# Kernel optimization log

Measured on AMD Instinct MI355X. Metric: run time of the kernel, lower is better.

Reference implementation:

```python
import jax, jax.numpy as jnp
import numpy as np

N, F_IN, HID, HEADS, NCLS, E = 50000, 512, 64, 4, 64, 800000
NEG_SLOPE = 0.2
EPS = 1e-16


def setup_inputs() -> dict:
    key = jax.random.key(0)
    ks = jax.random.split(key, 10)
    s = 0.1
    return {
        "x": jax.random.normal(ks[0], (N, F_IN), jnp.float32),
        "edge_index": jax.random.randint(ks[1], (2, E), 0, N, jnp.int64),
        "W1": jax.random.normal(ks[2], (F_IN, HEADS * HID), jnp.float32) * s,
        "a_src1": jax.random.normal(ks[3], (HEADS, HID), jnp.float32) * s,
        "a_dst1": jax.random.normal(ks[4], (HEADS, HID), jnp.float32) * s,
        "b1": jax.random.normal(ks[5], (HEADS * HID,), jnp.float32) * s,
        "W2": jax.random.normal(ks[6], (HEADS * HID, NCLS), jnp.float32) * s,
        "a_src2": jax.random.normal(ks[7], (1, NCLS), jnp.float32) * s,
        "a_dst2": jax.random.normal(ks[8], (1, NCLS), jnp.float32) * s,
        "b2": jax.random.normal(ks[9], (NCLS,), jnp.float32) * s,
    }


def gat_conv(x, W, a_src, a_dst, b, src, dst):
    H, C = a_src.shape
    h = (x @ W).reshape(-1, H, C)                     # [N, H, C]
    # per-node attention halves, gathered per edge -> [E', H]
    al_src = jnp.einsum("nhc,hc->nh", h, a_src)
    al_dst = jnp.einsum("nhc,hc->nh", h, a_dst)
    e = jax.nn.leaky_relu(al_src[src] + al_dst[dst], NEG_SLOPE)
    # segment softmax over destination neighborhoods
    m = jax.ops.segment_max(e, dst, num_segments=x.shape[0])
    ex = jnp.exp(e - m[dst])
    denom = jax.ops.segment_sum(ex, dst, num_segments=x.shape[0])
    alpha = ex / (denom[dst] + EPS)                   # [E', H]
    out = jax.ops.segment_sum(alpha[:, :, None] * h[src], dst,
                              num_segments=x.shape[0])  # [N, H, C]
    return out.reshape(-1, H * C) + b


def reference(x, edge_index, W1, a_src1, a_dst1, b1, W2, a_src2, a_dst2, b2):
    n = x.shape[0]
    loop = jnp.arange(n, dtype=edge_index.dtype)
    src = jnp.concatenate([edge_index[0], loop])       # add self loops (PyG default)
    dst = jnp.concatenate([edge_index[1], loop])
    h = gat_conv(x, W1, a_src1, a_dst1, b1, src, dst)
    h = jax.nn.elu(h)                                  # dropout is identity in eval
    out = gat_conv(h, W2, a_src2, a_dst2, b2, src, dst)
    return jax.nn.log_softmax(out, axis=1)
```

## Files before the change

### kernel.cpp

```cpp
#include <hip/hip_runtime.h>
#include <math.h>

#define F_IN 512
#define HC1 256
#define HEADS 4
#define HID 64
#define NCLS 64
#define NEG_SLOPE 0.2f
#define EPS_DENOM 1e-16f

using short8 = __attribute__((ext_vector_type(8))) short;
using f32x4  = __attribute__((ext_vector_type(4))) float;

__device__ inline float wave_sum(float v) {
#pragma unroll
  for (int s = 32; s > 0; s >>= 1) v += __shfl_xor(v, s);
  return v;
}

__device__ inline unsigned short f2bf(float f) {
  unsigned int u = __float_as_uint(f);
  u = (u + 0x7FFF + ((u >> 16) & 1)) >> 16;
  return (unsigned short)u;
}
__device__ inline float bflo(unsigned int u) { return __uint_as_float(u << 16); }
__device__ inline float bfhi(unsigned int u) { return __uint_as_float(u & 0xFFFF0000u); }

__device__ inline unsigned int cvtpk_bf16(float lo, float hi) {
  unsigned int r;
  asm("v_cvt_pk_bf16_f32 %0, %1, %2" : "=v"(r) : "v"(lo), "v"(hi));
  return r;
}

__device__ inline void async_copy16(const void* g, void* l) {
  __builtin_amdgcn_global_load_lds((const __attribute__((address_space(1))) void*)g,
                                   (__attribute__((address_space(3))) void*)l, 16, 0, 0);
}

__global__ void castT_kernel(const float* __restrict__ W, unsigned short* __restrict__ WT,
                             int K, int Nn) {
  int id = blockIdx.x * blockDim.x + threadIdx.x;
  if (id >= K * Nn) return;
  int n = id / K, k = id % K;
  WT[id] = f2bf(W[(size_t)k * Nn + n]);
}


__global__ void hist_kernel(const int* __restrict__ dst, int E, int* __restrict__ cnt) {
  int i = blockIdx.x * blockDim.x + threadIdx.x;
  int stride = gridDim.x * blockDim.x;
  for (int e = i; e < E; e += stride) atomicAdd(&cnt[dst[e]], 1);
}

__global__ void scan_blocks_kernel(const int* __restrict__ cnt, int n,
                                   int* __restrict__ rowoff, int* __restrict__ cursor,
                                   int* __restrict__ bsum) {
  __shared__ int wpart[16];
  int b = blockIdx.x, tid = threadIdx.x;
  int i = b * 1024 + tid;
  int lane = tid & 63, wid = tid >> 6;
  int v = (i < n) ? (cnt[i] + 1) : 0;
  int x = v;
#pragma unroll
  for (int s = 1; s < 64; s <<= 1) {
    int t = __shfl_up(x, s);
    if (lane >= s) x += t;
  }
  if (lane == 63) wpart[wid] = x;
  __syncthreads();
  if (wid == 0) {
    int p = (lane < 16) ? wpart[lane] : 0;
#pragma unroll
    for (int s = 1; s < 16; s <<= 1) {
      int t = __shfl_up(p, s);
      if (lane >= s) p += t;
    }
    if (lane < 16) wpart[lane] = p;
  }
  __syncthreads();
  int incl = x + (wid ? wpart[wid - 1] : 0);
  if (i < n) { rowoff[i + 1] = incl; cursor[i] = incl - v; }
  if (tid == 1023) bsum[b] = incl;
  if (b == 0 && tid == 0) rowoff[0] = 0;
}

__global__ void scan_partials_kernel(int* __restrict__ bsum, int nb) {
  int lane = threadIdx.x;
  int v = (lane < nb) ? bsum[lane] : 0;
  int x = v;
#pragma unroll
  for (int s = 1; s < 64; s <<= 1) {
    int t = __shfl_up(x, s);
    if (lane >= s) x += t;
  }
  if (lane < nb) bsum[lane] = x - v;
}

__global__ void scan_add_kernel(int n, int* __restrict__ rowoff, int* __restrict__ cursor,
                                const int* __restrict__ bsum) {
  int i = blockIdx.x * 1024 + threadIdx.x;
  int off = bsum[blockIdx.x];
  if (i < n) { rowoff[i + 1] += off; cursor[i] += off; }
}

__global__ void scatter_kernel(const int* __restrict__ src, const int* __restrict__ dst,
                               int E, int n, int* __restrict__ cursor, int* __restrict__ esrc) {
  int i = blockIdx.x * blockDim.x + threadIdx.x;
  int stride = gridDim.x * blockDim.x;
  for (int e = i; e < E + n; e += stride) {
    int s, d;
    if (e < E) { s = src[e]; d = dst[e]; } else { s = e - E; d = s; }
    int pos = atomicAdd(&cursor[d], 1);
    esrc[pos] = s;
  }
}


__global__ __launch_bounds__(256)
void gemm1_fused_kernel(const float* __restrict__ A, const unsigned short* __restrict__ BT,
                        unsigned short* __restrict__ Cb, int M) {
  constexpr int BM = 128, BN = 128, BK = 32, K = F_IN, Nn = HC1;
  __shared__ unsigned short Alds[BM * BK];
  __shared__ unsigned short Blds[BN * BK];
  const int t = threadIdx.x;
  const int lane = t & 63;
  const int w = t >> 6;
  const int wr = (w >> 1) * 64;
  const int wc = (w & 1) * 64;
  const int row0 = blockIdx.y * BM;
  const int col0 = blockIdx.x * BN;
  const int lrow = lane & 15;
  const int lk = (lane >> 4) * 8;

  f32x4 acc[4][4] = {};
  const int ar = t >> 1;
  const int kh = (t & 1) * 16;
  int grow = row0 + ar; if (grow > M - 1) grow = M - 1;
  const float* arow = A + (size_t)grow * K + kh;

  for (int k0 = 0; k0 < K; k0 += BK) {
#pragma unroll
    for (int i = 0; i < 2; ++i) {
      int c = i * 256 + t;
      int br = c >> 2;
      int bk = (c & 3) * 8;
      const unsigned short* g = BT + (size_t)(col0 + br) * K + k0 + bk;
      unsigned short* l = Blds + (size_t)(i * 256 + w * 64) * 8;
      async_copy16(g, l);
    }
    const float4* gp = (const float4*)(arow + k0);
    float4 f0 = gp[0], f1 = gp[1], f2 = gp[2], f3 = gp[3];
    uint4 u0, u1;
    u0.x = cvtpk_bf16(f0.x, f0.y); u0.y = cvtpk_bf16(f0.z, f0.w);
    u0.z = cvtpk_bf16(f1.x, f1.y); u0.w = cvtpk_bf16(f1.z, f1.w);
    u1.x = cvtpk_bf16(f2.x, f2.y); u1.y = cvtpk_bf16(f2.z, f2.w);
    u1.z = cvtpk_bf16(f3.x, f3.y); u1.w = cvtpk_bf16(f3.z, f3.w);
    uint4* dstp = (uint4*)&Alds[ar * BK + kh];
    dstp[0] = u0; dstp[1] = u1;
    __syncthreads();
    short8 a[4], b[4];
#pragma unroll
    for (int m = 0; m < 4; ++m)
      a[m] = *(const short8*)&Alds[(wr + m * 16 + lrow) * BK + lk];
#pragma unroll
    for (int n = 0; n < 4; ++n)
      b[n] = *(const short8*)&Blds[(wc + n * 16 + lrow) * BK + lk];
#pragma unroll
    for (int m = 0; m < 4; ++m)
#pragma unroll
      for (int n = 0; n < 4; ++n)
        acc[m][n] = __builtin_amdgcn_mfma_f32_16x16x32_bf16(a[m], b[n], acc[m][n], 0, 0, 0);
    __syncthreads();
  }
#pragma unroll
  for (int m = 0; m < 4; ++m) {
#pragma unroll
    for (int j = 0; j < 4; ++j) {
      int r = row0 + wr + m * 16 + (lane >> 4) * 4 + j;
      if (r < M) {
#pragma unroll
        for (int n = 0; n < 4; ++n)
          Cb[(size_t)r * Nn + col0 + wc + n * 16 + lrow] = f2bf(acc[m][n][j]);
      }
    }
  }
}


template <int BN>
__global__ __launch_bounds__(256)
void mfma_gemm_kernel(const unsigned short* __restrict__ A,
                      const unsigned short* __restrict__ BT,
                      unsigned short* __restrict__ Cb, int M, int Nn, int K) {
  constexpr int BM = 128, BK = 32;
  constexpr int NACC = BN / 32;
  __shared__ unsigned short Alds[BM * BK];
  __shared__ unsigned short Blds[BN * BK];
  const int t = threadIdx.x;
  const int lane = t & 63;
  const int w = t >> 6;
  const int wr = (w >> 1) * 64;
  const int wc = (w & 1) * (BN / 2);
  const int row0 = blockIdx.y * BM;
  const int col0 = blockIdx.x * BN;
  const int lrow = lane & 15;
  const int lk = (lane >> 4) * 8;

  f32x4 acc[4][NACC] = {};
  constexpr int AI = (BM * BK) / (256 * 8);
  constexpr int BI = (BN * BK) / (256 * 8);

  for (int k0 = 0; k0 < K; k0 += BK) {
#pragma unroll
    for (int i = 0; i < AI; ++i) {
      int c = i * 256 + t;
      int ar = c >> 2;
      int ak = (c & 3) * 8;
      int grow = row0 + ar; if (grow > M - 1) grow = M - 1;
      const unsigned short* g = A + (size_t)grow * K + k0 + ak;
      unsigned short* l = Alds + (size_t)(i * 256 + w * 64) * 8;
      async_copy16(g, l);
    }
#pragma unroll
    for (int i = 0; i < BI; ++i) {
      int c = i * 256 + t;
      int br = c >> 2;
      int bk = (c & 3) * 8;
      const unsigned short* g = BT + (size_t)(col0 + br) * K + k0 + bk;
      unsigned short* l = Blds + (size_t)(i * 256 + w * 64) * 8;
      async_copy16(g, l);
    }
    __syncthreads();
    short8 a[4], b[NACC];
#pragma unroll
    for (int m = 0; m < 4; ++m)
      a[m] = *(const short8*)&Alds[(wr + m * 16 + lrow) * BK + lk];
#pragma unroll
    for (int n = 0; n < NACC; ++n)
      b[n] = *(const short8*)&Blds[(wc + n * 16 + lrow) * BK + lk];
#pragma unroll
    for (int m = 0; m < 4; ++m)
#pragma unroll
      for (int n = 0; n < NACC; ++n)
        acc[m][n] = __builtin_amdgcn_mfma_f32_16x16x32_bf16(a[m], b[n], acc[m][n], 0, 0, 0);
    __syncthreads();
  }
#pragma unroll
  for (int m = 0; m < 4; ++m) {
#pragma unroll
    for (int j = 0; j < 4; ++j) {
      int r = row0 + wr + m * 16 + (lane >> 4) * 4 + j;
      if (r < M) {
#pragma unroll
        for (int n = 0; n < NACC; ++n)
          Cb[(size_t)r * Nn + col0 + wc + n * 16 + lrow] = f2bf(acc[m][n][j]);
      }
    }
  }
}


__global__ void attn1_kernel(const unsigned short* __restrict__ h1b,
                             const float* __restrict__ a_src, const float* __restrict__ a_dst,
                             float* __restrict__ als, float* __restrict__ ald, int n) {
  int w = threadIdx.x >> 6;
  int node = blockIdx.x * 4 + w;
  if (node >= n) return;
  int lane = threadIdx.x & 63;
  uint2 d = *(const uint2*)&h1b[(size_t)node * HC1 + lane * 4];
  float f0 = bflo(d.x), f1 = bfhi(d.x), f2 = bflo(d.y), f3 = bfhi(d.y);
  float4 as_ = ((const float4*)a_src)[lane];
  float4 ad_ = ((const float4*)a_dst)[lane];
  float ps = f0 * as_.x + f1 * as_.y + f2 * as_.z + f3 * as_.w;
  float pd = f0 * ad_.x + f1 * ad_.y + f2 * ad_.z + f3 * ad_.w;
#pragma unroll
  for (int s = 1; s < 16; s <<= 1) {
    ps += __shfl_xor(ps, s);
    pd += __shfl_xor(pd, s);
  }
  if ((lane & 15) == 0) {
    als[node * HEADS + (lane >> 4)] = ps;
    ald[node * HEADS + (lane >> 4)] = pd;
  }
}

__global__ void attn2_kernel(const unsigned short* __restrict__ h2b,
                             const float* __restrict__ a_src, const float* __restrict__ a_dst,
                             float* __restrict__ als, float* __restrict__ ald, int n) {
  int w = threadIdx.x >> 6;
  int node = blockIdx.x * 4 + w;
  if (node >= n) return;
  int lane = threadIdx.x & 63;
  float v = __uint_as_float(((unsigned int)h2b[(size_t)node * NCLS + lane]) << 16);
  float ps = wave_sum(v * a_src[lane]);
  float pd = wave_sum(v * a_dst[lane]);
  if (lane == 0) { als[node] = ps; ald[node] = pd; }
}


__global__ void agg1_kernel(const unsigned short* __restrict__ h1b,
                            const float4* __restrict__ als1, const float4* __restrict__ ald1,
                            const int* __restrict__ rowoff, const int* __restrict__ esrc,
                            const float* __restrict__ b1, unsigned short* __restrict__ hact,
                            int n) {
  __shared__ float wlds[4][256];
  __shared__ int   slds[4][64];
  int w = threadIdx.x >> 6;
  int node = blockIdx.x * 4 + w;
  if (node >= n) return;
  int lane = threadIdx.x & 63;
  int hi = lane >> 5;
  int cl = lane & 31;
  int head = cl >> 3;
  int beg = rowoff[node], end = rowoff[node + 1];
  float4 aldn = ald1[node];
  f32x4 accA = {0.f, 0.f, 0.f, 0.f};
  f32x4 accB = {0.f, 0.f, 0.f, 0.f};
  float dl0 = 0.f, dl1 = 0.f, dl2 = 0.f, dl3 = 0.f;

  for (int base = beg; base < end; base += 64) {
    int cnt = min(64, end - base);
    if (lane < cnt) {
      int s = esrc[base + lane];
      float4 av = als1[s];
      float v, w0, w1, w2, w3;
      v = av.x + aldn.x; v = fmaxf(v, NEG_SLOPE * v); w0 = __expf(v);
      v = av.y + aldn.y; v = fmaxf(v, NEG_SLOPE * v); w1 = __expf(v);
      v = av.z + aldn.z; v = fmaxf(v, NEG_SLOPE * v); w2 = __expf(v);
      v = av.w + aldn.w; v = fmaxf(v, NEG_SLOPE * v); w3 = __expf(v);
      dl0 += w0; dl1 += w1; dl2 += w2; dl3 += w3;
      slds[w][lane] = s;
      float4 wv = {w0, w1, w2, w3};
      *(float4*)&wlds[w][lane * 4] = wv;
    }

    uint4 dA[4], dB[4];
    float wA[4], wB[4];
    auto ISSUE = [&](int j0, uint4* d, float* wj) {
#pragma unroll
      for (int ii = 0; ii < 4; ++ii) {
        int e = j0 + 2 * ii + hi;
        bool val = e < cnt;
        int se = val ? e : 0;
        int ss = slds[w][se];
        wj[ii] = val ? wlds[w][se * 4 + head] : 0.f;
        d[ii] = *(const uint4*)&h1b[(size_t)ss * HC1 + cl * 8];
      }
    };
    auto CONSUME = [&](const uint4* d, const float* wj) {
#pragma unroll
      for (int ii = 0; ii < 4; ++ii) {
        float q = wj[ii];
        accA[0] += q * bflo(d[ii].x); accA[1] += q * bfhi(d[ii].x);
        accA[2] += q * bflo(d[ii].y); accA[3] += q * bfhi(d[ii].y);
        accB[0] += q * bflo(d[ii].z); accB[1] += q * bfhi(d[ii].z);
        accB[2] += q * bflo(d[ii].w); accB[3] += q * bfhi(d[ii].w);
      }
    };

    ISSUE(0, dA, wA);
    for (int j0 = 8;; j0 += 16) {
      bool hasB = j0 < cnt;
      if (hasB) ISSUE(j0, dB, wB);
      CONSUME(dA, wA);
      if (!hasB) break;
      bool hasA = (j0 + 8) < cnt;
      if (hasA) ISSUE(j0 + 8, dA, wA);
      CONSUME(dB, wB);
      if (!hasA) break;
    }
  }

#pragma unroll
  for (int k = 0; k < 4; ++k) {
    accA[k] += __shfl_xor(accA[k], 32);
    accB[k] += __shfl_xor(accB[k], 32);
  }
  float d0 = wave_sum(dl0), d1 = wave_sum(dl1);
  float d2 = wave_sum(dl2), d3 = wave_sum(dl3);
  float den = head < 2 ? (head == 0 ? d0 : d1) : (head == 2 ? d2 : d3);
  float rden = 1.f / (den + EPS_DENOM);
  if (hi == 0) {
    float4 bv0 = *(const float4*)&b1[cl * 8];
    float4 bv1 = *(const float4*)&b1[cl * 8 + 4];
    float o[8];
    o[0] = accA[0] * rden + bv0.x; o[1] = accA[1] * rden + bv0.y;
    o[2] = accA[2] * rden + bv0.z; o[3] = accA[3] * rden + bv0.w;
    o[4] = accB[0] * rden + bv1.x; o[5] = accB[1] * rden + bv1.y;
    o[6] = accB[2] * rden + bv1.z; o[7] = accB[3] * rden + bv1.w;
    ushort4 ov0, ov1;
#pragma unroll
    for (int k = 0; k < 8; ++k) o[k] = o[k] > 0.f ? o[k] : __expf(o[k]) - 1.f;
    ov0.x = f2bf(o[0]); ov0.y = f2bf(o[1]); ov0.z = f2bf(o[2]); ov0.w = f2bf(o[3]);
    ov1.x = f2bf(o[4]); ov1.y = f2bf(o[5]); ov1.z = f2bf(o[6]); ov1.w = f2bf(o[7]);
    *(ushort4*)&hact[(size_t)node * HC1 + cl * 8] = ov0;
    *(ushort4*)&hact[(size_t)node * HC1 + cl * 8 + 4] = ov1;
  }
}

__global__ void agg2_kernel(const unsigned short* __restrict__ h2b,
                            const float* __restrict__ als2, const float* __restrict__ ald2,
                            const int* __restrict__ rowoff, const int* __restrict__ esrc,
                            const float* __restrict__ b2, float* __restrict__ out, int n) {
  __shared__ float wlds[4][64];
  __shared__ int   slds[4][64];
  int w = threadIdx.x >> 6;
  int node = blockIdx.x * 4 + w;
  if (node >= n) return;
  int lane = threadIdx.x & 63;
  int eg = lane >> 3;
  int cl = lane & 7;
  int beg = rowoff[node], end = rowoff[node + 1];
  float aldn = ald2[node];
  f32x4 accA = {0.f, 0.f, 0.f, 0.f};
  f32x4 accB = {0.f, 0.f, 0.f, 0.f};
  float dl = 0.f;
  for (int base = beg; base < end; base += 64) {
    int cnt = min(64, end - base);
    if (lane < cnt) {
      int s = esrc[base + lane];
      float v = als2[s] + aldn;
      v = fmaxf(v, NEG_SLOPE * v);
      float wl = __expf(v);
      dl += wl;
      slds[w][lane] = s;
      wlds[w][lane] = wl;
    }
    for (int j0 = 0; j0 < cnt; j0 += 32) {
      uint4 d[4]; float wj[4];
#pragma unroll
      for (int ii = 0; ii < 4; ++ii) {
        int e = j0 + ii * 8 + eg;
        bool val = e < cnt;
        int se = val ? e : 0;
        int ss = slds[w][se];
        wj[ii] = val ? wlds[w][se] : 0.f;
        d[ii] = *(const uint4*)&h2b[(size_t)ss * NCLS + cl * 8];
      }
#pragma unroll
      for (int ii = 0; ii < 4; ++ii) {
        float q = wj[ii];
        accA[0] += q * bflo(d[ii].x); accA[1] += q * bfhi(d[ii].x);
        accA[2] += q * bflo(d[ii].y); accA[3] += q * bfhi(d[ii].y);
        accB[0] += q * bflo(d[ii].z); accB[1] += q * bfhi(d[ii].z);
        accB[2] += q * bflo(d[ii].w); accB[3] += q * bfhi(d[ii].w);
      }
    }
  }
#pragma unroll
  for (int s = 8; s < 64; s <<= 1) {
#pragma unroll
    for (int k = 0; k < 4; ++k) {
      accA[k] += __shfl_xor(accA[k], s);
      accB[k] += __shfl_xor(accB[k], s);
    }
  }
  float den = wave_sum(dl);
  float rden = 1.f / (den + EPS_DENOM);
  float4 bv0 = *(const float4*)&b2[cl * 8];
  float4 bv1 = *(const float4*)&b2[cl * 8 + 4];
  float o[8];
  o[0] = accA[0] * rden + bv0.x; o[1] = accA[1] * rden + bv0.y;
  o[2] = accA[2] * rden + bv0.z; o[3] = accA[3] * rden + bv0.w;
  o[4] = accB[0] * rden + bv1.x; o[5] = accB[1] * rden + bv1.y;
  o[6] = accB[2] * rden + bv1.z; o[7] = accB[3] * rden + bv1.w;
  float mx = o[0];
#pragma unroll
  for (int k = 1; k < 8; ++k) mx = fmaxf(mx, o[k]);
#pragma unroll
  for (int s = 1; s < 8; s <<= 1) mx = fmaxf(mx, __shfl_xor(mx, s));
  float sm = 0.f;
#pragma unroll
  for (int k = 0; k < 8; ++k) sm += __expf(o[k] - mx);
#pragma unroll
  for (int s = 1; s < 8; s <<= 1) sm += __shfl_xor(sm, s);
  float ls = mx + __logf(sm);
  if (lane < 8) {
    float4 q0 = {o[0] - ls, o[1] - ls, o[2] - ls, o[3] - ls};
    float4 q1 = {o[4] - ls, o[5] - ls, o[6] - ls, o[7] - ls};
    *(float4*)&out[(size_t)node * NCLS + cl * 8] = q0;
    *(float4*)&out[(size_t)node * NCLS + cl * 8 + 4] = q1;
  }
}


extern "C" void kernel_launch(void* const* d_in, const int* in_sizes, int n_in,
                              void* d_out, int out_size, void* d_ws, size_t ws_size,
                              hipStream_t stream) {
  const float* x      = (const float*)d_in[0];
  const int*   eidx   = (const int*)d_in[1];
  const float* W1     = (const float*)d_in[2];
  const float* a_src1 = (const float*)d_in[3];
  const float* a_dst1 = (const float*)d_in[4];
  const float* b1     = (const float*)d_in[5];
  const float* W2     = (const float*)d_in[6];
  const float* a_src2 = (const float*)d_in[7];
  const float* a_dst2 = (const float*)d_in[8];
  const float* b2     = (const float*)d_in[9];
  float* out = (float*)d_out;

  const int Nn = in_sizes[0] / F_IN;
  const int E  = in_sizes[1] / 2;
  const int* esrc_in = eidx;
  const int* edst_in = eidx + E;

  char* ws = (char*)d_ws;
  size_t off = 0;
  auto alloc = [&](size_t bytes) -> void* {
    void* p = ws + off;
    off += (bytes + 255) & ~(size_t)255;
    return p;
  };
  unsigned short* h1b    = (unsigned short*)alloc((size_t)Nn * HC1 * sizeof(short));
  unsigned short* hact   = (unsigned short*)alloc((size_t)Nn * HC1 * sizeof(short));
  unsigned short* h2b    = (unsigned short*)alloc((size_t)Nn * NCLS * sizeof(short));
  unsigned short* W1T    = (unsigned short*)alloc((size_t)F_IN * HC1 * sizeof(short));
  unsigned short* W2T    = (unsigned short*)alloc((size_t)HC1 * NCLS * sizeof(short));
  float*          als1   = (float*)alloc((size_t)Nn * HEADS * sizeof(float));
  float*          ald1   = (float*)alloc((size_t)Nn * HEADS * sizeof(float));
  float*          als2   = (float*)alloc((size_t)Nn * sizeof(float));
  float*          ald2   = (float*)alloc((size_t)Nn * sizeof(float));
  int*            cnt    = (int*)alloc((size_t)Nn * sizeof(int));
  int*            rowoff = (int*)alloc((size_t)(Nn + 1) * sizeof(int));
  int*            cursor = (int*)alloc((size_t)Nn * sizeof(int));
  int*            bsum   = (int*)alloc(256 * sizeof(int));
  int*            esrc   = (int*)alloc((size_t)(E + Nn) * sizeof(int));

  const int nscan = (Nn + 1023) / 1024;

  castT_kernel<<<(F_IN * HC1 + 255) / 256, 256, 0, stream>>>(W1, W1T, F_IN, HC1);
  castT_kernel<<<(HC1 * NCLS + 255) / 256, 256, 0, stream>>>(W2, W2T, HC1, NCLS);

  hipMemsetAsync(cnt, 0, (size_t)Nn * sizeof(int), stream);
  hist_kernel<<<(E + 255) / 256, 256, 0, stream>>>(edst_in, E, cnt);
  scan_blocks_kernel<<<nscan, 1024, 0, stream>>>(cnt, Nn, rowoff, cursor, bsum);
  scan_partials_kernel<<<1, 64, 0, stream>>>(bsum, nscan);
  scan_add_kernel<<<nscan, 1024, 0, stream>>>(Nn, rowoff, cursor, bsum);
  scatter_kernel<<<(E + Nn + 255) / 256, 256, 0, stream>>>(esrc_in, edst_in, E, Nn, cursor, esrc);

  {
    dim3 g(HC1 / 128, (Nn + 127) / 128);
    gemm1_fused_kernel<<<g, 256, 0, stream>>>(x, W1T, h1b, Nn);
  }
  {
    int blocks = (Nn + 3) / 4;
    attn1_kernel<<<blocks, 256, 0, stream>>>(h1b, a_src1, a_dst1, als1, ald1, Nn);
    agg1_kernel<<<blocks, 256, 0, stream>>>(h1b, (const float4*)als1, (const float4*)ald1,
                                            rowoff, esrc, b1, hact, Nn);
  }

  {
    dim3 g(NCLS / 64, (Nn + 127) / 128);
    mfma_gemm_kernel<64><<<g, 256, 0, stream>>>(hact, W2T, h2b, Nn, NCLS, HC1);
  }
  {
    int blocks = (Nn + 3) / 4;
    attn2_kernel<<<blocks, 256, 0, stream>>>(h2b, a_src2, a_dst2, als2, ald2, Nn);
    agg2_kernel<<<blocks, 256, 0, stream>>>(h2b, als2, ald2, rowoff, esrc, b2, out, Nn);
  }
}
```

Measured before the change: 279.5 us.

## Fuse attention-logit dot products into both GEMM epilogues and double-buffer GEMM1

Both GEMMs now compute the per-node source and destination attention logits in their epilogue using fp32 accumulators, so the two separate attention kernels and their re-reads of h1/h2 are removed. GEMM1 widens to one 128x256 tile per block with 512 threads, so x is read once instead of once per column half. It also double-buffers the A and B LDS tiles, prefetching the next k-slice while the current one runs on MFMA. GEMM2 uses one block per row tile and combines the two wave halves' partial sums with shared-memory atomics. The costs are higher LDS and register use per block in GEMM1, fewer blocks, and logits taken from fp32 accumulators rather than the bf16-rounded values.

```diff
diff --git a/kernel.cpp b/kernel.cpp
--- a/kernel.cpp
+++ b/kernel.cpp
@@ -116,185 +116,206 @@
 }
 
 
+__global__ __launch_bounds__(512)
+void gemm1_fused_kernel(const float* __restrict__ A, const unsigned short* __restrict__ BT,
+                        unsigned short* __restrict__ Cb,
+                        const float* __restrict__ as1, const float* __restrict__ ad1,
+                        float* __restrict__ als, float* __restrict__ ald, int M) {
+  constexpr int BM = 128, BN = 256, BK = 32, K = F_IN, Nn = HC1;
+  __shared__ unsigned short Alds[2][BM * BK];
+  __shared__ unsigned short Blds[2][BN * BK];
+  const int t = threadIdx.x;
+  const int lane = t & 63;
+  const int w = t >> 6;
+  const int wr = (w >> 2) * 64;
+  const int wc = (w & 3) * 64;
+  const int head = w & 3;
+  const int row0 = blockIdx.x * BM;
+  const int lrow = lane & 15;
+  const int lk = (lane >> 4) * 8;
+
+  f32x4 acc[4][4] = {};
+
+  const int ar = t >> 2, kq = (t & 3) * 8;
+  int grow = row0 + ar; if (grow > M - 1) grow = M - 1;
+  const float* aptr = A + (size_t)grow * K + kq;
+
+  float4 fa0, fa1;
+  fa0 = *(const float4*)(aptr);
+  fa1 = *(const float4*)(aptr + 4);
+#pragma unroll
+  for (int i = 0; i < 2; ++i) {
+    int c = i * 512 + t;
+    const unsigned short* g = BT + (size_t)(c >> 2) * K + (c & 3) * 8;
+    async_copy16(g, &Blds[0][(size_t)c * 8]);
+  }
+  {
+    uint4 u;
+    u.x = cvtpk_bf16(fa0.x, fa0.y); u.y = cvtpk_bf16(fa0.z, fa0.w);
+    u.z = cvtpk_bf16(fa1.x, fa1.y); u.w = cvtpk_bf16(fa1.z, fa1.w);
+    *(uint4*)&Alds[0][ar * BK + kq] = u;
+  }
+  int cur = 0;
+  for (int k0 = 0; k0 < K; k0 += BK) {
+    __syncthreads();
+    const int nxt = cur ^ 1;
+    const bool more = (k0 + BK) < K;
+    if (more) {
+#pragma unroll
+      for (int i = 0; i < 2; ++i) {
+        int c = i * 512 + t;
+        const unsigned short* g = BT + (size_t)(c >> 2) * K + (k0 + BK) + (c & 3) * 8;
+        async_copy16(g, &Blds[nxt][(size_t)c * 8]);
+      }
+      fa0 = *(const float4*)(aptr + k0 + BK);
+      fa1 = *(const float4*)(aptr + k0 + BK + 4);
+    }
+    short8 a[4], b[4];
+#pragma unroll
+    for (int m = 0; m < 4; ++m)
+      a[m] = *(const short8*)&Alds[cur][(wr + m * 16 + lrow) * BK + lk];
+#pragma unroll
+    for (int n = 0; n < 4; ++n)
+      b[n] = *(const short8*)&Blds[cur][(wc + n * 16 + lrow) * BK + lk];
+#pragma unroll
+    for (int m = 0; m < 4; ++m)
+#pragma unroll
+      for (int n = 0; n < 4; ++n)
+        acc[m][n] = __builtin_amdgcn_mfma_f32_16x16x32_bf16(a[m], b[n], acc[m][n], 0, 0, 0);
+    if (more) {
+      uint4 u;
+      u.x = cvtpk_bf16(fa0.x, fa0.y); u.y = cvtpk_bf16(fa0.z, fa0.w);
+      u.z = cvtpk_bf16(fa1.x, fa1.y); u.w = cvtpk_bf16(fa1.z, fa1.w);
+      *(uint4*)&Alds[nxt][ar * BK + kq] = u;
+    }
+    cur = nxt;
+  }
+
+  float asv[4], adv[4];
+#pragma unroll
+  for (int n = 0; n < 4; ++n) {
+    asv[n] = as1[head * 64 + n * 16 + lrow];
+    adv[n] = ad1[head * 64 + n * 16 + lrow];
+  }
+#pragma unroll
+  for (int m = 0; m < 4; ++m) {
+#pragma unroll
+    for (int j = 0; j < 4; ++j) {
+      int r = row0 + wr + m * 16 + (lane >> 4) * 4 + j;
+      float ps = 0.f, pd = 0.f;
+#pragma unroll
+      for (int n = 0; n < 4; ++n) {
+        float v = acc[m][n][j];
+        ps += v * asv[n];
+        pd += v * adv[n];
+        if (r < M) Cb[(size_t)r * Nn + wc + n * 16 + lrow] = f2bf(v);
+      }
+#pragma unroll
+      for (int s = 1; s < 16; s <<= 1) {
+        ps += __shfl_xor(ps, s);
+        pd += __shfl_xor(pd, s);
+      }
+      if ((lane & 15) == 0 && r < M) {
+        als[r * HEADS + head] = ps;
+        ald[r * HEADS + head] = pd;
+      }
+    }
+  }
+}
+
+
 __global__ __launch_bounds__(256)
-void gemm1_fused_kernel(const float* __restrict__ A, const unsigned short* __restrict__ BT,
-                        unsigned short* __restrict__ Cb, int M) {
-  constexpr int BM = 128, BN = 128, BK = 32, K = F_IN, Nn = HC1;
+void gemm2_fused_kernel(const unsigned short* __restrict__ A,
+                        const unsigned short* __restrict__ BT,
+                        unsigned short* __restrict__ Cb,
+                        const float* __restrict__ as2, const float* __restrict__ ad2,
+                        float* __restrict__ als, float* __restrict__ ald, int M) {
+  constexpr int BM = 128, BN = 64, BK = 32, K = HC1, Nn = NCLS;
   __shared__ unsigned short Alds[BM * BK];
   __shared__ unsigned short Blds[BN * BK];
+  __shared__ float sps[BM], spd[BM];
   const int t = threadIdx.x;
   const int lane = t & 63;
   const int w = t >> 6;
   const int wr = (w >> 1) * 64;
-  const int wc = (w & 1) * 64;
-  const int row0 = blockIdx.y * BM;
-  const int col0 = blockIdx.x * BN;
+  const int wc = (w & 1) * 32;
+  const int row0 = blockIdx.x * BM;
   const int lrow = lane & 15;
   const int lk = (lane >> 4) * 8;
-
-  f32x4 acc[4][4] = {};
-  const int ar = t >> 1;
-  const int kh = (t & 1) * 16;
-  int grow = row0 + ar; if (grow > M - 1) grow = M - 1;
-  const float* arow = A + (size_t)grow * K + kh;
-
+  if (t < BM) { sps[t] = 0.f; spd[t] = 0.f; }
+
+  f32x4 acc[4][2] = {};
   for (int k0 = 0; k0 < K; k0 += BK) {
 #pragma unroll
     for (int i = 0; i < 2; ++i) {
       int c = i * 256 + t;
-      int br = c >> 2;
-      int bk = (c & 3) * 8;
-      const unsigned short* g = BT + (size_t)(col0 + br) * K + k0 + bk;
-      unsigned short* l = Blds + (size_t)(i * 256 + w * 64) * 8;
-      async_copy16(g, l);
-    }
-    const float4* gp = (const float4*)(arow + k0);
-    float4 f0 = gp[0], f1 = gp[1], f2 = gp[2], f3 = gp[3];
-    uint4 u0, u1;
-    u0.x = cvtpk_bf16(f0.x, f0.y); u0.y = cvtpk_bf16(f0.z, f0.w);
-    u0.z = cvtpk_bf16(f1.x, f1.y); u0.w = cvtpk_bf16(f1.z, f1.w);
-    u1.x = cvtpk_bf16(f2.x, f2.y); u1.y = cvtpk_bf16(f2.z, f2.w);
-    u1.z = cvtpk_bf16(f3.x, f3.y); u1.w = cvtpk_bf16(f3.z, f3.w);
-    uint4* dstp = (uint4*)&Alds[ar * BK + kh];
-    dstp[0] = u0; dstp[1] = u1;
-    __syncthreads();
-    short8 a[4], b[4];
-#pragma unroll
-    for (int m = 0; m < 4; ++m)
-      a[m] = *(const short8*)&Alds[(wr + m * 16 + lrow) * BK + lk];
-#pragma unroll
-    for (int n = 0; n < 4; ++n)
-      b[n] = *(const short8*)&Blds[(wc + n * 16 + lrow) * BK + lk];
-#pragma unroll
-    for (int m = 0; m < 4; ++m)
-#pragma unroll
-      for (int n = 0; n < 4; ++n)
-        acc[m][n] = __builtin_amdgcn_mfma_f32_16x16x32_bf16(a[m], b[n], acc[m][n], 0, 0, 0);
-    __syncthreads();
-  }
-#pragma unroll
-  for (int m = 0; m < 4; ++m) {
-#pragma unroll
-    for (int j = 0; j < 4; ++j) {
-      int r = row0 + wr + m * 16 + (lane >> 4) * 4 + j;
-      if (r < M) {
-#pragma unroll
-        for (int n = 0; n < 4; ++n)
-          Cb[(size_t)r * Nn + col0 + wc + n * 16 + lrow] = f2bf(acc[m][n][j]);
-      }
-    }
-  }
-}
-
-
-template <int BN>
-__global__ __launch_bounds__(256)
-void mfma_gemm_kernel(const unsigned short* __restrict__ A,
-                      const unsigned short* __restrict__ BT,
-                      unsigned short* __restrict__ Cb, int M, int Nn, int K) {
-  constexpr int BM = 128, BK = 32;
-  constexpr int NACC = BN / 32;
-  __shared__ unsigned short Alds[BM * BK];
-  __shared__ unsigned short Blds[BN * BK];
-  const int t = threadIdx.x;
-  const int lane = t & 63;
-  const int w = t >> 6;
-  const int wr = (w >> 1) * 64;
-  const int wc = (w & 1) * (BN / 2);
-  const int row0 = blockIdx.y * BM;
-  const int col0 = blockIdx.x * BN;
-  const int lrow = lane & 15;
-  const int lk = (lane >> 4) * 8;
-
-  f32x4 acc[4][NACC] = {};
-  constexpr int AI = (BM * BK) / (256 * 8);
-  constexpr int BI = (BN * BK) / (256 * 8);
-
-  for (int k0 = 0; k0 < K; k0 += BK) {
-#pragma unroll
-    for (int i = 0; i < AI; ++i) {
-      int c = i * 256 + t;
-      int ar = c >> 2;
+      int arr = c >> 2;
       int ak = (c & 3) * 8;
-      int grow = row0 + ar; if (grow > M - 1) grow = M - 1;
+      int grow = row0 + arr; if (grow > M - 1) grow = M - 1;
       const unsigned short* g = A + (size_t)grow * K + k0 + ak;
       unsigned short* l = Alds + (size_t)(i * 256 + w * 64) * 8;
       async_copy16(g, l);
     }
-#pragma unroll
-    for (int i = 0; i < BI; ++i) {
-      int c = i * 256 + t;
+    {
+      int c = t;
       int br = c >> 2;
       int bk = (c & 3) * 8;
-      const unsigned short* g = BT + (size_t)(col0 + br) * K + k0 + bk;
-      unsigned short* l = Blds + (size_t)(i * 256 + w * 64) * 8;
+      const unsigned short* g = BT + (size_t)br * K + k0 + bk;
+      unsigned short* l = Blds + (size_t)(w * 64) * 8;
       async_copy16(g, l);
     }
     __syncthreads();
-    short8 a[4], b[NACC];
+    short8 a[4], b[2];
 #pragma unroll
     for (int m = 0; m < 4; ++m)
       a[m] = *(const short8*)&Alds[(wr + m * 16 + lrow) * BK + lk];
 #pragma unroll
-    for (int n = 0; n < NACC; ++n)
+    for (int n = 0; n < 2; ++n)
       b[n] = *(const short8*)&Blds[(wc + n * 16 + lrow) * BK + lk];
 #pragma unroll
     for (int m = 0; m < 4; ++m)
 #pragma unroll
-      for (int n = 0; n < NACC; ++n)
+      for (int n = 0; n < 2; ++n)
         acc[m][n] = __builtin_amdgcn_mfma_f32_16x16x32_bf16(a[m], b[n], acc[m][n], 0, 0, 0);
     __syncthreads();
   }
+
+  float asv[2], adv[2];
+#pragma unroll
+  for (int n = 0; n < 2; ++n) {
+    asv[n] = as2[wc + n * 16 + lrow];
+    adv[n] = ad2[wc + n * 16 + lrow];
+  }
 #pragma unroll
   for (int m = 0; m < 4; ++m) {
 #pragma unroll
     for (int j = 0; j < 4; ++j) {
-      int r = row0 + wr + m * 16 + (lane >> 4) * 4 + j;
-      if (r < M) {
-#pragma unroll
-        for (int n = 0; n < NACC; ++n)
-          Cb[(size_t)r * Nn + col0 + wc + n * 16 + lrow] = f2bf(acc[m][n][j]);
-      }
-    }
-  }
-}
-
-
-__global__ void attn1_kernel(const unsigned short* __restrict__ h1b,
-                             const float* __restrict__ a_src, const float* __restrict__ a_dst,
-                             float* __restrict__ als, float* __restrict__ ald, int n) {
-  int w = threadIdx.x >> 6;
-  int node = blockIdx.x * 4 + w;
-  if (node >= n) return;
-  int lane = threadIdx.x & 63;
-  uint2 d = *(const uint2*)&h1b[(size_t)node * HC1 + lane * 4];
-  float f0 = bflo(d.x), f1 = bfhi(d.x), f2 = bflo(d.y), f3 = bfhi(d.y);
-  float4 as_ = ((const float4*)a_src)[lane];
-  float4 ad_ = ((const float4*)a_dst)[lane];
-  float ps = f0 * as_.x + f1 * as_.y + f2 * as_.z + f3 * as_.w;
-  float pd = f0 * ad_.x + f1 * ad_.y + f2 * ad_.z + f3 * ad_.w;
-#pragma unroll
-  for (int s = 1; s < 16; s <<= 1) {
-    ps += __shfl_xor(ps, s);
-    pd += __shfl_xor(pd, s);
-  }
-  if ((lane & 15) == 0) {
-    als[node * HEADS + (lane >> 4)] = ps;
-    ald[node * HEADS + (lane >> 4)] = pd;
-  }
-}
-
-__global__ void attn2_kernel(const unsigned short* __restrict__ h2b,
-                             const float* __restrict__ a_src, const float* __restrict__ a_dst,
-                             float* __restrict__ als, float* __restrict__ ald, int n) {
-  int w = threadIdx.x >> 6;
-  int node = blockIdx.x * 4 + w;
-  if (node >= n) return;
-  int lane = threadIdx.x & 63;
-  float v = __uint_as_float(((unsigned int)h2b[(size_t)node * NCLS + lane]) << 16);
-  float ps = wave_sum(v * a_src[lane]);
-  float pd = wave_sum(v * a_dst[lane]);
-  if (lane == 0) { als[node] = ps; ald[node] = pd; }
+      int rl = wr + m * 16 + (lane >> 4) * 4 + j;
+      int r = row0 + rl;
+      float ps = 0.f, pd = 0.f;
+#pragma unroll
+      for (int n = 0; n < 2; ++n) {
+        float v = acc[m][n][j];
+        ps += v * asv[n];
+        pd += v * adv[n];
+        if (r < M) Cb[(size_t)r * Nn + wc + n * 16 + lrow] = f2bf(v);
+      }
+#pragma unroll
+      for (int s = 1; s < 16; s <<= 1) {
+        ps += __shfl_xor(ps, s);
+        pd += __shfl_xor(pd, s);
+      }
+      if ((lane & 15) == 0) {
+        atomicAdd(&sps[rl], ps);
+        atomicAdd(&spd[rl], pd);
+      }
+    }
+  }
+  __syncthreads();
+  if (t < BM) {
+    int r = row0 + t;
+    if (r < M) { als[r] = sps[t]; ald[r] = spd[t]; }
+  }
 }
 
 
@@ -539,23 +560,19 @@
   scatter_kernel<<<(E + Nn + 255) / 256, 256, 0, stream>>>(esrc_in, edst_in, E, Nn, cursor, esrc);
 
   {
-    dim3 g(HC1 / 128, (Nn + 127) / 128);
-    gemm1_fused_kernel<<<g, 256, 0, stream>>>(x, W1T, h1b, Nn);
-  }
+    int blocks = (Nn + 127) / 128;
+    gemm1_fused_kernel<<<blocks, 512, 0, stream>>>(x, W1T, h1b, a_src1, a_dst1,
+                                                   als1, ald1, Nn);
+    int ablocks = (Nn + 3) / 4;
+    agg1_kernel<<<ablocks, 256, 0, stream>>>(h1b, (const float4*)als1, (const float4*)ald1,
+                                             rowoff, esrc, b1, hact, Nn);
+  }
+
   {
-    int blocks = (Nn + 3) / 4;
-    attn1_kernel<<<blocks, 256, 0, stream>>>(h1b, a_src1, a_dst1, als1, ald1, Nn);
-    agg1_kernel<<<blocks, 256, 0, stream>>>(h1b, (const float4*)als1, (const float4*)ald1,
-                                            rowoff, esrc, b1, hact, Nn);
-  }
-
-  {
-    dim3 g(NCLS / 64, (Nn + 127) / 128);
-    mfma_gemm_kernel<64><<<g, 256, 0, stream>>>(hact, W2T, h2b, Nn, NCLS, HC1);
-  }
-  {
-    int blocks = (Nn + 3) / 4;
-    attn2_kernel<<<blocks, 256, 0, stream>>>(h2b, a_src2, a_dst2, als2, ald2, Nn);
-    agg2_kernel<<<blocks, 256, 0, stream>>>(h2b, als2, ald2, rowoff, esrc, b2, out, Nn);
-  }
-}
+    int blocks = (Nn + 127) / 128;
+    gemm2_fused_kernel<<<blocks, 256, 0, stream>>>(hact, W2T, h2b, a_src2, a_dst2,
+                                                   als2, ald2, Nn);
+    int ablocks = (Nn + 3) / 4;
+    agg2_kernel<<<ablocks, 256, 0, stream>>>(h2b, als2, ald2, rowoff, esrc, b2, out, Nn);
+  }
+}
```

Result: faster. 261.4 us (-6.5%).
